# Performance work log

Hardware: AMD Instinct MI355X
Metric: run time of the kernel (lower is better)

## Reference

```python
import jax, jax.numpy as jnp
import numpy as np

N_HEAD = 8
D_HEAD = 64
D_MODEL = 512
CTX = 64
B = 2
Q_LEN = 2048
T = Q_LEN + CTX - 1


def setup_inputs() -> dict:
    key = jax.random.key(0)
    ks = jax.random.split(key, 7)
    HD = N_HEAD * D_HEAD
    return {
        "x": jax.random.normal(ks[0], (B, T, D_MODEL), jnp.float32),
        "r": jax.random.normal(ks[1], (CTX, D_MODEL), jnp.float32),
        "Wkv": jax.random.normal(ks[2], (D_MODEL, 2 * HD), jnp.float32) * 0.02,
        "Wq": jax.random.normal(ks[3], (D_MODEL, HD), jnp.float32) * 0.02,
        "bq": jax.random.normal(ks[4], (HD,), jnp.float32) * 0.02,
        "Wr": jax.random.normal(ks[5], (D_MODEL, HD), jnp.float32) * 0.02,
        "Wo": jax.random.normal(ks[6], (HD, D_MODEL), jnp.float32) * 0.02,
    }


def reference(x, r, Wkv, Wq, bq, Wr, Wo):
    Bb, Tt, _ = x.shape
    C = r.shape[0]
    H, Dh = N_HEAD, D_HEAD
    q_len = Tt - C + 1
    scale = Dh ** -0.5

    kv = x @ Wkv                                  # [B, T, 2*H*Dh]
    k_all = kv[..., : H * Dh].reshape(Bb, Tt, H, Dh)
    v_all = kv[..., H * Dh:].reshape(Bb, Tt, H, Dh)

    # sliding windows (torch unfold(1, ctx, 1) equivalent)
    idx = jnp.arange(q_len)[:, None] + jnp.arange(C)[None, :]   # [q, C]
    k_win = k_all[:, idx]                         # [B, q, C, H, Dh]
    v_win = v_all[:, idx]                         # [B, q, C, H, Dh]

    hq = (x[:, C - 1:] @ Wq + bq).reshape(Bb, q_len, H, Dh)     # [B, q, H, Dh]
    hr = (r @ Wr).reshape(C, H, Dh)                              # [C, H, Dh]

    # q . (k + r): split into content term + relative-position bias term
    scores = (jnp.einsum('bqhd,bqchd->bhqc', hq, k_win)
              + jnp.einsum('bqhd,chd->bhqc', hq, hr)) * scale    # [B, H, q, C]

    # padding mask: positions in first ctx-1 steps that are all-zero
    pad_mask = jnp.all(x[:, : C - 1] == 0, axis=-1)              # [B, C-1]
    full_mask = jnp.concatenate(
        [pad_mask, jnp.zeros((Bb, q_len), dtype=bool)], axis=1)  # [B, T]
    mask_win = full_mask[:, idx]                                 # [B, q, C]
    scores = jnp.where(mask_win[:, None], -jnp.inf, scores)

    w = jax.nn.softmax(scores, axis=-1)                          # [B, H, q, C]
    out = jnp.einsum('bhqc,bqchd->bqhd', w, v_win).reshape(Bb, q_len, H * Dh)
    return out @ Wo                                              # [B, q, d_model]
```

## Files before the change

kernel.cpp:

```cpp
#include <hip/hip_runtime.h>
#include <cstdint>
#include <cstddef>

#define NH 8
#define DH 64
#define DM 512
#define CTX 64
#define BB 2
#define QL 2048
#define TT (QL + CTX - 1)
#define HDIM 512
#define KVN 1024
#define KD 512

typedef unsigned short u16;
typedef __attribute__((ext_vector_type(8))) short bf16x8;
typedef __attribute__((ext_vector_type(4))) float f32x4;

__device__ __forceinline__ u16 f2bf(float f) {
    uint32_t u = __float_as_uint(f);
    u += 0x7FFF + ((u >> 16) & 1);
    return (u16)(u >> 16);
}
__device__ __forceinline__ float bf2f(u16 u) {
    return __uint_as_float((uint32_t)u << 16);
}

#define GLLDS(g, l) __builtin_amdgcn_global_load_lds( \
    (const __attribute__((address_space(1))) void*)(g), \
    (__attribute__((address_space(3))) void*)(l), 16, 0, 0)

__global__ __launch_bounds__(256) void prep_kernel(
    const float* __restrict__ x, const float* __restrict__ r,
    const float* __restrict__ Wkv, const float* __restrict__ Wq,
    const float* __restrict__ Wr, const float* __restrict__ Wo,
    u16* __restrict__ xb, u16* __restrict__ rb, u16* __restrict__ WkvqT,
    u16* __restrict__ WrT, u16* __restrict__ WoT, float* __restrict__ maskv)
{
    __shared__ float tile[64][65];
    __shared__ int anyflag;
    int bid = blockIdx.x;
    const int tid = threadIdx.x;

    if (bid < 2111) {
        int i = bid * 256 + tid;
        float4 v = ((const float4*)x)[i];
        ushort4 o; o.x = f2bf(v.x); o.y = f2bf(v.y); o.z = f2bf(v.z); o.w = f2bf(v.w);
        ((ushort4*)xb)[i] = o;
        return;
    }
    bid -= 2111;
    if (bid < 32) {
        int i = bid * 256 + tid;
        float4 v = ((const float4*)r)[i];
        ushort4 o; o.x = f2bf(v.x); o.y = f2bf(v.y); o.z = f2bf(v.z); o.w = f2bf(v.w);
        ((ushort4*)rb)[i] = o;
        return;
    }
    bid -= 32;
    if (bid >= 320) {
        int idx = bid - 320;
        int t = idx >> 1, b = idx & 1;
        const float* row = x + (size_t)(b * TT + t) * DM;
        bool nz = (row[tid] != 0.f) || (row[tid + 256] != 0.f);
        if (tid == 0) anyflag = 0;
        __syncthreads();
        unsigned long long bal = __ballot(nz);
        if ((tid & 63) == 0 && bal) atomicOr(&anyflag, 1);
        __syncthreads();
        if (tid == 0) maskv[b * 64 + t] = anyflag ? 0.f : -1e30f;
        return;
    }
    const float* W; u16* WT; int N; int tidx;
    if (bid < 128)      { W = Wkv; WT = WkvqT;                    N = 1024; tidx = bid; }
    else if (bid < 192) { W = Wq;  WT = WkvqT + (size_t)1024*512; N = 512;  tidx = bid - 128; }
    else if (bid < 256) { W = Wr;  WT = WrT;                      N = 512;  tidx = bid - 192; }
    else                { W = Wo;  WT = WoT;                      N = 512;  tidx = bid - 256; }
    const int tpr = N / 64;
    const int kb = (tidx / tpr) * 64, nb = (tidx % tpr) * 64;
    const int c4 = (tid & 15) * 4;
    for (int kk = tid >> 4; kk < 64; kk += 16) {
        float4 v = *(const float4*)&W[(size_t)(kb + kk) * N + nb + c4];
        tile[kk][c4 + 0] = v.x; tile[kk][c4 + 1] = v.y;
        tile[kk][c4 + 2] = v.z; tile[kk][c4 + 3] = v.w;
    }
    __syncthreads();
    for (int nn = tid >> 4; nn < 64; nn += 16) {
        ushort4 o;
        o.x = f2bf(tile[c4 + 0][nn]); o.y = f2bf(tile[c4 + 1][nn]);
        o.z = f2bf(tile[c4 + 2][nn]); o.w = f2bf(tile[c4 + 3][nn]);
        *(ushort4*)&WT[(size_t)(nb + nn) * KD + kb + c4] = o;
    }
}

__global__ __launch_bounds__(256) void gemm_mfma(
    const u16* __restrict__ A, const u16* __restrict__ BT,
    u16* __restrict__ C, u16* __restrict__ C2, const float* __restrict__ bq,
    int mode)
{
    __shared__ u16 As[128 * 32];
    __shared__ u16 Bs[128 * 32];

    const int tid  = threadIdx.x;
    const int lane = tid & 63;
    const int w    = tid >> 6;
    const int wm   = (w >> 1) * 64;
    const int wn   = (w & 1) * 64;
    const int m0   = blockIdx.y * 128;
    const int n0   = blockIdx.x * 128;

    const int am0 = tid >> 2;
    const int ak0 = (tid & 3) * 8;
    const u16* ga0 = A  + (size_t)(m0 + am0) * KD + ak0;
    const u16* ga1 = ga0 + (size_t)64 * KD;
    const u16* gb0 = BT + (size_t)(n0 + am0) * KD + ak0;
    const u16* gb1 = gb0 + (size_t)64 * KD;

    f32x4 acc[4][4];
#pragma unroll
    for (int i = 0; i < 4; i++)
#pragma unroll
        for (int j = 0; j < 4; j++)
            acc[i][j] = (f32x4){0.f, 0.f, 0.f, 0.f};

    for (int kt = 0; kt < KD; kt += 32) {
        __syncthreads();
        GLLDS(ga0 + kt, &As[(size_t)w * 512]);
        GLLDS(ga1 + kt, &As[2048 + (size_t)w * 512]);
        GLLDS(gb0 + kt, &Bs[(size_t)w * 512]);
        GLLDS(gb1 + kt, &Bs[2048 + (size_t)w * 512]);
        __syncthreads();

        const int fm = lane & 15;
        const int fk = (lane >> 4) * 8;
        bf16x8 af[4], bfr[4];
#pragma unroll
        for (int i = 0; i < 4; i++)
            af[i] = *(const bf16x8*)&As[(wm + i * 16 + fm) * 32 + fk];
#pragma unroll
        for (int j = 0; j < 4; j++)
            bfr[j] = *(const bf16x8*)&Bs[(wn + j * 16 + fm) * 32 + fk];
#pragma unroll
        for (int i = 0; i < 4; i++)
#pragma unroll
            for (int j = 0; j < 4; j++)
                acc[i][j] = __builtin_amdgcn_mfma_f32_16x16x32_bf16(af[i], bfr[j], acc[i][j], 0, 0, 0);
    }

    const int fc = lane & 15;
    const int fr = (lane >> 4) * 4;
    if (mode == 1) {
        const bool iskv = (n0 < 1024);
#pragma unroll
        for (int i = 0; i < 4; i++)
#pragma unroll
            for (int rr = 0; rr < 4; rr++) {
                int row = m0 + wm + i * 16 + fr + rr;
                if (row < BB * TT) {
                    if (iskv) {
#pragma unroll
                        for (int j = 0; j < 4; j++) {
                            int col = n0 + wn + j * 16 + fc;
                            C[(size_t)row * KVN + col] = f2bf(acc[i][j][rr]);
                        }
                    } else {
                        int bb = row / TT;
                        int t  = row - bb * TT;
                        if (t >= CTX - 1) {
                            size_t orow = (size_t)(bb * QL + t - (CTX - 1));
#pragma unroll
                            for (int j = 0; j < 4; j++) {
                                int col = n0 + wn + j * 16 + fc - 1024;
                                C2[orow * HDIM + col] = f2bf(acc[i][j][rr] + bq[col]);
                            }
                        }
                    }
                }
            }
    } else {
#pragma unroll
        for (int i = 0; i < 4; i++)
#pragma unroll
            for (int rr = 0; rr < 4; rr++) {
                int row = m0 + wm + i * 16 + fr + rr;
                if (row < CTX) {
#pragma unroll
                    for (int j = 0; j < 4; j++) {
                        int col = n0 + wn + j * 16 + fc;
                        C[(size_t)row * HDIM + col] = f2bf(acc[i][j][rr]);
                    }
                }
            }
    }
}

__global__ __launch_bounds__(256) void gemm_n64(
    const u16* __restrict__ A, const u16* __restrict__ BT,
    float* __restrict__ C, int M, int N)
{
    __shared__ u16 As[128 * 32];
    __shared__ u16 Bs[64 * 32];

    const int tid  = threadIdx.x;
    const int lane = tid & 63;
    const int w    = tid >> 6;
    const int wm   = (w >> 1) * 64;
    const int wn   = (w & 1) * 32;
    const int m0   = blockIdx.y * 128;
    const int n0   = blockIdx.x * 64;

    const int am0 = tid >> 2;
    const int ak0 = (tid & 3) * 8;
    const u16* ga0 = A  + (size_t)(m0 + am0) * KD + ak0;
    const u16* ga1 = ga0 + (size_t)64 * KD;
    const u16* gb0 = BT + (size_t)(n0 + am0) * KD + ak0;

    f32x4 acc[4][2];
#pragma unroll
    for (int i = 0; i < 4; i++)
#pragma unroll
        for (int j = 0; j < 2; j++)
            acc[i][j] = (f32x4){0.f, 0.f, 0.f, 0.f};

    for (int kt = 0; kt < KD; kt += 32) {
        __syncthreads();
        GLLDS(ga0 + kt, &As[(size_t)w * 512]);
        GLLDS(ga1 + kt, &As[2048 + (size_t)w * 512]);
        GLLDS(gb0 + kt, &Bs[(size_t)w * 512]);
        __syncthreads();

        const int fm = lane & 15;
        const int fk = (lane >> 4) * 8;
        bf16x8 af[4], bfr[2];
#pragma unroll
        for (int i = 0; i < 4; i++)
            af[i] = *(const bf16x8*)&As[(wm + i * 16 + fm) * 32 + fk];
#pragma unroll
        for (int j = 0; j < 2; j++)
            bfr[j] = *(const bf16x8*)&Bs[(wn + j * 16 + fm) * 32 + fk];
#pragma unroll
        for (int i = 0; i < 4; i++)
#pragma unroll
            for (int j = 0; j < 2; j++)
                acc[i][j] = __builtin_amdgcn_mfma_f32_16x16x32_bf16(af[i], bfr[j], acc[i][j], 0, 0, 0);
    }

    const int fc = lane & 15;
    const int fr = (lane >> 4) * 4;
#pragma unroll
    for (int i = 0; i < 4; i++)
#pragma unroll
        for (int rr = 0; rr < 4; rr++) {
            int row = m0 + wm + i * 16 + fr + rr;
            if (row < M) {
#pragma unroll
                for (int j = 0; j < 2; j++) {
                    int col = n0 + wn + j * 16 + fc;
                    C[(size_t)row * N + col] = acc[i][j][rr];
                }
            }
        }
}

__global__ __launch_bounds__(256) void attn_mfma(
    const u16* __restrict__ kvb, const u16* __restrict__ hqb,
    const u16* __restrict__ hrb, const float* __restrict__ maskv,
    u16* __restrict__ attnb)
{
    __shared__ __align__(16) char lds[55296];
    float* sprime = (float*)lds;
    u16*   vTs    = (u16*)lds;
    float* s2s    = (float*)(lds + 20480);
    u16*   wband  = (u16*)(lds + 37888);

    const int q0 = blockIdx.x * 64;
    const int h  = blockIdx.y;
    const int b  = blockIdx.z;
    const int tid  = threadIdx.x;
    const int lane = tid & 63;
    const int w    = tid >> 6;
    const int qb   = q0 + w * 16;

    {
        uint32_t* wz = (uint32_t*)wband;
#pragma unroll
        for (int i = 0; i < 17; i++) wz[tid + i * 256] = 0;
    }
    __syncthreads();

    const int fm = lane & 15;
    const int fk = (lane >> 4) * 8;

    const u16* hqrow = hqb + (size_t)(b * QL + qb + fm) * HDIM + h * DH + fk;
    bf16x8 afr0 = *(const bf16x8*)(hqrow);
    bf16x8 afr1 = *(const bf16x8*)(hqrow + 32);

    {
        const u16* kbase = kvb + (size_t)(b * TT + qb + fm) * KVN + h * DH + fk;
#pragma unroll
        for (int nt = 0; nt < 5; nt++) {
            bf16x8 b0 = *(const bf16x8*)(kbase + (size_t)nt * 16 * KVN);
            bf16x8 b1 = *(const bf16x8*)(kbase + (size_t)nt * 16 * KVN + 32);
            f32x4 acc = (f32x4){0.f, 0.f, 0.f, 0.f};
            acc = __builtin_amdgcn_mfma_f32_16x16x32_bf16(afr0, b0, acc, 0, 0, 0);
            acc = __builtin_amdgcn_mfma_f32_16x16x32_bf16(afr1, b1, acc, 0, 0, 0);
            const int row = (lane >> 4) * 4;
#pragma unroll
            for (int r = 0; r < 4; r++)
                sprime[w * 1280 + (row + r) * 80 + nt * 16 + fm] = acc[r];
        }
    }
    {
        const u16* hrbase = hrb + (size_t)fm * HDIM + h * DH + fk;
#pragma unroll
        for (int nc = 0; nc < 4; nc++) {
            bf16x8 b0 = *(const bf16x8*)(hrbase + (size_t)nc * 16 * HDIM);
            bf16x8 b1 = *(const bf16x8*)(hrbase + (size_t)nc * 16 * HDIM + 32);
            f32x4 acc = (f32x4){0.f, 0.f, 0.f, 0.f};
            acc = __builtin_amdgcn_mfma_f32_16x16x32_bf16(afr0, b0, acc, 0, 0, 0);
            acc = __builtin_amdgcn_mfma_f32_16x16x32_bf16(afr1, b1, acc, 0, 0, 0);
            const int row = (lane >> 4) * 4;
#pragma unroll
            for (int r = 0; r < 4; r++)
                s2s[w * 1088 + (row + r) * 68 + nc * 16 + fm] = acc[r];
        }
    }

#pragma unroll 1
    for (int i = 0; i < 16; i++) {
        const int qloc = w * 16 + i;
        float s = (sprime[w * 1280 + i * 80 + i + lane] +
                   s2s[w * 1088 + i * 68 + lane]) * 0.125f;
        if (q0 == 0) {
            int t = qloc + lane;
            if (t < 63) s += maskv[b * 64 + t];
        }
        float mx = s;
#pragma unroll
        for (int off = 32; off; off >>= 1) mx = fmaxf(mx, __shfl_xor(mx, off, 64));
        float e = __expf(s - mx);
        float sum = e;
#pragma unroll
        for (int off = 32; off; off >>= 1) sum += __shfl_xor(sum, off, 64);
        wband[qloc * 136 + qloc + lane] = f2bf(e / sum);
    }
    __syncthreads();

    {
        const int r0 = tid >> 4;
        const int c4 = (tid & 15) * 4;
        for (int rr = r0; rr < 127; rr += 16) {
            ushort4 vv = *(const ushort4*)&kvb[(size_t)(b * TT + q0 + rr) * KVN + HDIM + h * DH + c4];
            vTs[(c4 + 0) * 136 + rr] = vv.x;
            vTs[(c4 + 1) * 136 + rr] = vv.y;
            vTs[(c4 + 2) * 136 + rr] = vv.z;
            vTs[(c4 + 3) * 136 + rr] = vv.w;
        }
        if (tid < 64) vTs[tid * 136 + 127] = 0;
    }
    __syncthreads();

    f32x4 oacc[4];
#pragma unroll
    for (int j = 0; j < 4; j++) oacc[j] = (f32x4){0.f, 0.f, 0.f, 0.f};
#pragma unroll
    for (int ks = 0; ks < 4; ks++) {
        bf16x8 wa = *(const bf16x8*)&wband[(w * 16 + fm) * 136 + ks * 32 + fk];
#pragma unroll
        for (int j = 0; j < 4; j++) {
            bf16x8 vb = *(const bf16x8*)&vTs[(j * 16 + fm) * 136 + ks * 32 + fk];
            oacc[j] = __builtin_amdgcn_mfma_f32_16x16x32_bf16(wa, vb, oacc[j], 0, 0, 0);
        }
    }
    {
        const int row = (lane >> 4) * 4;
#pragma unroll
        for (int j = 0; j < 4; j++)
#pragma unroll
            for (int r = 0; r < 4; r++)
                attnb[(size_t)(b * QL + qb + row + r) * HDIM + h * DH + j * 16 + fm] =
                    f2bf(oacc[j][r]);
    }
}

extern "C" void kernel_launch(void* const* d_in, const int* in_sizes, int n_in,
                              void* d_out, int out_size, void* d_ws, size_t ws_size,
                              hipStream_t stream)
{
    const float* x   = (const float*)d_in[0];
    const float* r   = (const float*)d_in[1];
    const float* Wkv = (const float*)d_in[2];
    const float* Wq  = (const float*)d_in[3];
    const float* bq  = (const float*)d_in[4];
    const float* Wr  = (const float*)d_in[5];
    const float* Wo  = (const float*)d_in[6];
    float* out = (float*)d_out;

    char* p = (char*)d_ws;
    u16* xb     = (u16*)p;  p += (size_t)4224 * 512 * 2;
    u16* rb     = (u16*)p;  p += (size_t)128 * 512 * 2;
    u16* WkvqT  = (u16*)p;  p += (size_t)1536 * 512 * 2;
    u16* WrT    = (u16*)p;  p += (size_t)512 * 512 * 2;
    u16* WoT    = (u16*)p;  p += (size_t)512 * 512 * 2;
    u16* kvb    = (u16*)p;  p += (size_t)4224 * 1024 * 2;
    u16* hqb    = (u16*)p;  p += (size_t)4096 * 512 * 2;
    u16* hrb    = (u16*)p;  p += (size_t)64 * 512 * 2;
    u16* attnb  = (u16*)p;  p += (size_t)4096 * 512 * 2;
    float* maskv = (float*)p;

    hipLaunchKernelGGL(prep_kernel, dim3(2589), dim3(256), 0, stream,
                       x, r, Wkv, Wq, Wr, Wo, xb, rb, WkvqT, WrT, WoT, maskv);
    hipLaunchKernelGGL(gemm_mfma, dim3(1536 / 128, 33), dim3(256), 0, stream,
                       xb, WkvqT, kvb, hqb, bq, 1);
    hipLaunchKernelGGL(gemm_mfma, dim3(512 / 128, 1), dim3(256), 0, stream,
                       rb, WrT, hrb, nullptr, nullptr, 2);
    hipLaunchKernelGGL(attn_mfma, dim3(QL / 64, NH, BB), dim3(256), 0, stream,
                       kvb, hqb, hrb, maskv, attnb);
    hipLaunchKernelGGL(gemm_n64, dim3(512 / 64, 4096 / 128), dim3(256), 0, stream,
                       attnb, WoT, out, 4096, 512);
}
```

Measured before the change: 133.6 us.

## Fuse all stages into one persistent cooperative kernel with grid syncs

Replaces the five separate launches (prep, QKV GEMM, hr GEMM, attention, output GEMM) with a single cooperative persistent kernel. Work is spread over blocks in grid-stride loops, and stages are separated by grid-wide barriers. The projection GEMM now uses a 128x64 tile instead of 128x128, which gives more work units to balance across the persistent grid, and the hr GEMM is folded into the same stage. The aim is to remove launch gaps and per-kernel tail effects. In exchange it pays for grid-sync overhead, and every stage runs at the occupancy allowed by the attention stage's 55 KB LDS footprint.

```diff
diff --git a/kernel.cpp b/kernel.cpp
--- a/kernel.cpp
+++ b/kernel.cpp
@@ -1,4 +1,5 @@
 #include <hip/hip_runtime.h>
+#include <hip/hip_cooperative_groups.h>
 #include <cstdint>
 #include <cstddef>
 
@@ -22,128 +23,61 @@
     u += 0x7FFF + ((u >> 16) & 1);
     return (u16)(u >> 16);
 }
-__device__ __forceinline__ float bf2f(u16 u) {
-    return __uint_as_float((uint32_t)u << 16);
-}
 
 #define GLLDS(g, l) __builtin_amdgcn_global_load_lds( \
     (const __attribute__((address_space(1))) void*)(g), \
     (__attribute__((address_space(3))) void*)(l), 16, 0, 0)
 
-__global__ __launch_bounds__(256) void prep_kernel(
-    const float* __restrict__ x, const float* __restrict__ r,
-    const float* __restrict__ Wkv, const float* __restrict__ Wq,
-    const float* __restrict__ Wr, const float* __restrict__ Wo,
-    u16* __restrict__ xb, u16* __restrict__ rb, u16* __restrict__ WkvqT,
-    u16* __restrict__ WrT, u16* __restrict__ WoT, float* __restrict__ maskv)
-{
-    __shared__ float tile[64][65];
-    __shared__ int anyflag;
-    int bid = blockIdx.x;
-    const int tid = threadIdx.x;
-
-    if (bid < 2111) {
-        int i = bid * 256 + tid;
-        float4 v = ((const float4*)x)[i];
-        ushort4 o; o.x = f2bf(v.x); o.y = f2bf(v.y); o.z = f2bf(v.z); o.w = f2bf(v.w);
-        ((ushort4*)xb)[i] = o;
-        return;
-    }
-    bid -= 2111;
-    if (bid < 32) {
-        int i = bid * 256 + tid;
-        float4 v = ((const float4*)r)[i];
-        ushort4 o; o.x = f2bf(v.x); o.y = f2bf(v.y); o.z = f2bf(v.z); o.w = f2bf(v.w);
-        ((ushort4*)rb)[i] = o;
-        return;
-    }
-    bid -= 32;
-    if (bid >= 320) {
-        int idx = bid - 320;
-        int t = idx >> 1, b = idx & 1;
-        const float* row = x + (size_t)(b * TT + t) * DM;
-        bool nz = (row[tid] != 0.f) || (row[tid + 256] != 0.f);
-        if (tid == 0) anyflag = 0;
-        __syncthreads();
-        unsigned long long bal = __ballot(nz);
-        if ((tid & 63) == 0 && bal) atomicOr(&anyflag, 1);
-        __syncthreads();
-        if (tid == 0) maskv[b * 64 + t] = anyflag ? 0.f : -1e30f;
-        return;
-    }
-    const float* W; u16* WT; int N; int tidx;
-    if (bid < 128)      { W = Wkv; WT = WkvqT;                    N = 1024; tidx = bid; }
-    else if (bid < 192) { W = Wq;  WT = WkvqT + (size_t)1024*512; N = 512;  tidx = bid - 128; }
-    else if (bid < 256) { W = Wr;  WT = WrT;                      N = 512;  tidx = bid - 192; }
-    else                { W = Wo;  WT = WoT;                      N = 512;  tidx = bid - 256; }
-    const int tpr = N / 64;
-    const int kb = (tidx / tpr) * 64, nb = (tidx % tpr) * 64;
-    const int c4 = (tid & 15) * 4;
-    for (int kk = tid >> 4; kk < 64; kk += 16) {
-        float4 v = *(const float4*)&W[(size_t)(kb + kk) * N + nb + c4];
-        tile[kk][c4 + 0] = v.x; tile[kk][c4 + 1] = v.y;
-        tile[kk][c4 + 2] = v.z; tile[kk][c4 + 3] = v.w;
-    }
-    __syncthreads();
-    for (int nn = tid >> 4; nn < 64; nn += 16) {
-        ushort4 o;
-        o.x = f2bf(tile[c4 + 0][nn]); o.y = f2bf(tile[c4 + 1][nn]);
-        o.z = f2bf(tile[c4 + 2][nn]); o.w = f2bf(tile[c4 + 3][nn]);
-        *(ushort4*)&WT[(size_t)(nb + nn) * KD + kb + c4] = o;
-    }
-}
-
-__global__ __launch_bounds__(256) void gemm_mfma(
+struct Ptrs {
+    const float *x, *r, *Wkv, *Wq, *bq, *Wr, *Wo;
+    float* outp;
+    u16 *xb, *rb, *WkvqT, *WrT, *WoT, *kvb, *hqb, *hrb, *attnb;
+    float* maskv;
+};
+
+__device__ __forceinline__ void gemm_unit(
     const u16* __restrict__ A, const u16* __restrict__ BT,
-    u16* __restrict__ C, u16* __restrict__ C2, const float* __restrict__ bq,
-    int mode)
-{
-    __shared__ u16 As[128 * 32];
-    __shared__ u16 Bs[128 * 32];
-
-    const int tid  = threadIdx.x;
+    int m0, int n0, char* smem, int tid, int mode, const Ptrs& p)
+{
+    u16* As = (u16*)smem;
+    u16* Bs = (u16*)(smem + 8192);
     const int lane = tid & 63;
     const int w    = tid >> 6;
     const int wm   = (w >> 1) * 64;
-    const int wn   = (w & 1) * 64;
-    const int m0   = blockIdx.y * 128;
-    const int n0   = blockIdx.x * 128;
-
-    const int am0 = tid >> 2;
-    const int ak0 = (tid & 3) * 8;
-    const u16* ga0 = A  + (size_t)(m0 + am0) * KD + ak0;
+    const int wn   = (w & 1) * 32;
+
+    const u16* ga0 = A  + (size_t)(m0 + (tid >> 2)) * KD + (tid & 3) * 8;
     const u16* ga1 = ga0 + (size_t)64 * KD;
-    const u16* gb0 = BT + (size_t)(n0 + am0) * KD + ak0;
-    const u16* gb1 = gb0 + (size_t)64 * KD;
-
-    f32x4 acc[4][4];
+    const u16* gb0 = BT + (size_t)(n0 + (tid >> 2)) * KD + (tid & 3) * 8;
+
+    f32x4 acc[4][2];
 #pragma unroll
     for (int i = 0; i < 4; i++)
 #pragma unroll
-        for (int j = 0; j < 4; j++)
+        for (int j = 0; j < 2; j++)
             acc[i][j] = (f32x4){0.f, 0.f, 0.f, 0.f};
+
+    const int fm = lane & 15;
+    const int fk = (lane >> 4) * 8;
 
     for (int kt = 0; kt < KD; kt += 32) {
         __syncthreads();
-        GLLDS(ga0 + kt, &As[(size_t)w * 512]);
-        GLLDS(ga1 + kt, &As[2048 + (size_t)w * 512]);
-        GLLDS(gb0 + kt, &Bs[(size_t)w * 512]);
-        GLLDS(gb1 + kt, &Bs[2048 + (size_t)w * 512]);
+        GLLDS(ga0 + kt, As + w * 512);
+        GLLDS(ga1 + kt, As + 2048 + w * 512);
+        GLLDS(gb0 + kt, Bs + w * 512);
         __syncthreads();
 
-        const int fm = lane & 15;
-        const int fk = (lane >> 4) * 8;
-        bf16x8 af[4], bfr[4];
+        bf16x8 af[4], bfr[2];
 #pragma unroll
         for (int i = 0; i < 4; i++)
             af[i] = *(const bf16x8*)&As[(wm + i * 16 + fm) * 32 + fk];
 #pragma unroll
-        for (int j = 0; j < 4; j++)
+        for (int j = 0; j < 2; j++)
             bfr[j] = *(const bf16x8*)&Bs[(wn + j * 16 + fm) * 32 + fk];
 #pragma unroll
         for (int i = 0; i < 4; i++)
 #pragma unroll
-            for (int j = 0; j < 4; j++)
+            for (int j = 0; j < 2; j++)
                 acc[i][j] = __builtin_amdgcn_mfma_f32_16x16x32_bf16(af[i], bfr[j], acc[i][j], 0, 0, 0);
     }
 
@@ -159,9 +93,9 @@
                 if (row < BB * TT) {
                     if (iskv) {
 #pragma unroll
-                        for (int j = 0; j < 4; j++) {
+                        for (int j = 0; j < 2; j++) {
                             int col = n0 + wn + j * 16 + fc;
-                            C[(size_t)row * KVN + col] = f2bf(acc[i][j][rr]);
+                            p.kvb[(size_t)row * KVN + col] = f2bf(acc[i][j][rr]);
                         }
                     } else {
                         int bb = row / TT;
@@ -169,15 +103,15 @@
                         if (t >= CTX - 1) {
                             size_t orow = (size_t)(bb * QL + t - (CTX - 1));
 #pragma unroll
-                            for (int j = 0; j < 4; j++) {
+                            for (int j = 0; j < 2; j++) {
                                 int col = n0 + wn + j * 16 + fc - 1024;
-                                C2[orow * HDIM + col] = f2bf(acc[i][j][rr] + bq[col]);
+                                p.hqb[orow * HDIM + col] = f2bf(acc[i][j][rr] + p.bq[col]);
                             }
                         }
                     }
                 }
             }
-    } else {
+    } else if (mode == 2) {
 #pragma unroll
         for (int i = 0; i < 4; i++)
 #pragma unroll
@@ -185,102 +119,109 @@
                 int row = m0 + wm + i * 16 + fr + rr;
                 if (row < CTX) {
 #pragma unroll
-                    for (int j = 0; j < 4; j++) {
+                    for (int j = 0; j < 2; j++) {
                         int col = n0 + wn + j * 16 + fc;
-                        C[(size_t)row * HDIM + col] = f2bf(acc[i][j][rr]);
+                        p.hrb[(size_t)row * HDIM + col] = f2bf(acc[i][j][rr]);
                     }
                 }
             }
-    }
-}
-
-__global__ __launch_bounds__(256) void gemm_n64(
-    const u16* __restrict__ A, const u16* __restrict__ BT,
-    float* __restrict__ C, int M, int N)
-{
-    __shared__ u16 As[128 * 32];
-    __shared__ u16 Bs[64 * 32];
-
-    const int tid  = threadIdx.x;
-    const int lane = tid & 63;
-    const int w    = tid >> 6;
-    const int wm   = (w >> 1) * 64;
-    const int wn   = (w & 1) * 32;
-    const int m0   = blockIdx.y * 128;
-    const int n0   = blockIdx.x * 64;
-
-    const int am0 = tid >> 2;
-    const int ak0 = (tid & 3) * 8;
-    const u16* ga0 = A  + (size_t)(m0 + am0) * KD + ak0;
-    const u16* ga1 = ga0 + (size_t)64 * KD;
-    const u16* gb0 = BT + (size_t)(n0 + am0) * KD + ak0;
-
-    f32x4 acc[4][2];
-#pragma unroll
-    for (int i = 0; i < 4; i++)
-#pragma unroll
-        for (int j = 0; j < 2; j++)
-            acc[i][j] = (f32x4){0.f, 0.f, 0.f, 0.f};
-
-    for (int kt = 0; kt < KD; kt += 32) {
-        __syncthreads();
-        GLLDS(ga0 + kt, &As[(size_t)w * 512]);
-        GLLDS(ga1 + kt, &As[2048 + (size_t)w * 512]);
-        GLLDS(gb0 + kt, &Bs[(size_t)w * 512]);
-        __syncthreads();
-
-        const int fm = lane & 15;
-        const int fk = (lane >> 4) * 8;
-        bf16x8 af[4], bfr[2];
+    } else {
 #pragma unroll
         for (int i = 0; i < 4; i++)
-            af[i] = *(const bf16x8*)&As[(wm + i * 16 + fm) * 32 + fk];
-#pragma unroll
-        for (int j = 0; j < 2; j++)
-            bfr[j] = *(const bf16x8*)&Bs[(wn + j * 16 + fm) * 32 + fk];
-#pragma unroll
-        for (int i = 0; i < 4; i++)
-#pragma unroll
-            for (int j = 0; j < 2; j++)
-                acc[i][j] = __builtin_amdgcn_mfma_f32_16x16x32_bf16(af[i], bfr[j], acc[i][j], 0, 0, 0);
-    }
-
-    const int fc = lane & 15;
-    const int fr = (lane >> 4) * 4;
-#pragma unroll
-    for (int i = 0; i < 4; i++)
-#pragma unroll
-        for (int rr = 0; rr < 4; rr++) {
-            int row = m0 + wm + i * 16 + fr + rr;
-            if (row < M) {
+#pragma unroll
+            for (int rr = 0; rr < 4; rr++) {
+                int row = m0 + wm + i * 16 + fr + rr;
 #pragma unroll
                 for (int j = 0; j < 2; j++) {
                     int col = n0 + wn + j * 16 + fc;
-                    C[(size_t)row * N + col] = acc[i][j][rr];
+                    p.outp[(size_t)row * DM + col] = acc[i][j][rr];
                 }
             }
-        }
-}
-
-__global__ __launch_bounds__(256) void attn_mfma(
-    const u16* __restrict__ kvb, const u16* __restrict__ hqb,
-    const u16* __restrict__ hrb, const float* __restrict__ maskv,
-    u16* __restrict__ attnb)
-{
-    __shared__ __align__(16) char lds[55296];
-    float* sprime = (float*)lds;
-    u16*   vTs    = (u16*)lds;
-    float* s2s    = (float*)(lds + 20480);
-    u16*   wband  = (u16*)(lds + 37888);
-
-    const int q0 = blockIdx.x * 64;
-    const int h  = blockIdx.y;
-    const int b  = blockIdx.z;
-    const int tid  = threadIdx.x;
+    }
+}
+
+__device__ __forceinline__ void stageA(int u, int tid, char* smem, const Ptrs& p)
+{
+    int bid = u;
+    if (bid < 2111) {
+        int i = bid * 256 + tid;
+        float4 v = ((const float4*)p.x)[i];
+        ushort4 o; o.x = f2bf(v.x); o.y = f2bf(v.y); o.z = f2bf(v.z); o.w = f2bf(v.w);
+        ((ushort4*)p.xb)[i] = o;
+        return;
+    }
+    bid -= 2111;
+    if (bid < 32) {
+        int i = bid * 256 + tid;
+        float4 v = ((const float4*)p.r)[i];
+        ushort4 o; o.x = f2bf(v.x); o.y = f2bf(v.y); o.z = f2bf(v.z); o.w = f2bf(v.w);
+        ((ushort4*)p.rb)[i] = o;
+        return;
+    }
+    bid -= 32;
+    if (bid >= 320) {
+        int* anyflag = (int*)(smem + 16896);
+        int idx = bid - 320;
+        int t = idx >> 1, b = idx & 1;
+        const float* row = p.x + (size_t)(b * TT + t) * DM;
+        bool nz = (row[tid] != 0.f) || (row[tid + 256] != 0.f);
+        if (tid == 0) *anyflag = 0;
+        __syncthreads();
+        unsigned long long bal = __ballot(nz);
+        if ((tid & 63) == 0 && bal) atomicOr(anyflag, 1);
+        __syncthreads();
+        if (tid == 0) p.maskv[b * 64 + t] = *anyflag ? 0.f : -1e30f;
+        return;
+    }
+    float (*tile)[65] = (float(*)[65])smem;
+    const float* W; u16* WT; int N; int tidx;
+    if (bid < 128)      { W = p.Wkv; WT = p.WkvqT;                      N = 1024; tidx = bid; }
+    else if (bid < 192) { W = p.Wq;  WT = p.WkvqT + (size_t)1024 * 512; N = 512;  tidx = bid - 128; }
+    else if (bid < 256) { W = p.Wr;  WT = p.WrT;                        N = 512;  tidx = bid - 192; }
+    else                { W = p.Wo;  WT = p.WoT;                        N = 512;  tidx = bid - 256; }
+    const int tpr = N / 64;
+    const int kb = (tidx / tpr) * 64, nbo = (tidx % tpr) * 64;
+    const int c4 = (tid & 15) * 4;
+    __syncthreads();
+    for (int kk = tid >> 4; kk < 64; kk += 16) {
+        float4 v = *(const float4*)&W[(size_t)(kb + kk) * N + nbo + c4];
+        tile[kk][c4 + 0] = v.x; tile[kk][c4 + 1] = v.y;
+        tile[kk][c4 + 2] = v.z; tile[kk][c4 + 3] = v.w;
+    }
+    __syncthreads();
+    for (int nn = tid >> 4; nn < 64; nn += 16) {
+        ushort4 o;
+        o.x = f2bf(tile[c4 + 0][nn]); o.y = f2bf(tile[c4 + 1][nn]);
+        o.z = f2bf(tile[c4 + 2][nn]); o.w = f2bf(tile[c4 + 3][nn]);
+        *(ushort4*)&WT[(size_t)(nbo + nn) * KD + kb + c4] = o;
+    }
+}
+
+__device__ __forceinline__ void stageB(int u, int tid, char* smem, const Ptrs& p)
+{
+    if (u < 792) {
+        int mu = u / 24, nu = u - mu * 24;
+        gemm_unit(p.xb, p.WkvqT, mu * 128, nu * 64, smem, tid, 1, p);
+    } else {
+        gemm_unit(p.rb, p.WrT, 0, (u - 792) * 64, smem, tid, 2, p);
+    }
+}
+
+__device__ __forceinline__ void stageC(int u, int tid, char* smem, const Ptrs& p)
+{
+    float* sprime = (float*)smem;
+    u16*   vTs    = (u16*)smem;
+    float* s2s    = (float*)(smem + 20480);
+    u16*   wband  = (u16*)(smem + 37888);
+
+    const int q0 = (u & 31) * 64;
+    const int h  = (u >> 5) & 7;
+    const int b  = u >> 8;
     const int lane = tid & 63;
     const int w    = tid >> 6;
     const int qb   = q0 + w * 16;
 
+    __syncthreads();
     {
         uint32_t* wz = (uint32_t*)wband;
 #pragma unroll
@@ -291,12 +232,12 @@
     const int fm = lane & 15;
     const int fk = (lane >> 4) * 8;
 
-    const u16* hqrow = hqb + (size_t)(b * QL + qb + fm) * HDIM + h * DH + fk;
+    const u16* hqrow = p.hqb + (size_t)(b * QL + qb + fm) * HDIM + h * DH + fk;
     bf16x8 afr0 = *(const bf16x8*)(hqrow);
     bf16x8 afr1 = *(const bf16x8*)(hqrow + 32);
 
     {
-        const u16* kbase = kvb + (size_t)(b * TT + qb + fm) * KVN + h * DH + fk;
+        const u16* kbase = p.kvb + (size_t)(b * TT + qb + fm) * KVN + h * DH + fk;
 #pragma unroll
         for (int nt = 0; nt < 5; nt++) {
             bf16x8 b0 = *(const bf16x8*)(kbase + (size_t)nt * 16 * KVN);
@@ -306,12 +247,12 @@
             acc = __builtin_amdgcn_mfma_f32_16x16x32_bf16(afr1, b1, acc, 0, 0, 0);
             const int row = (lane >> 4) * 4;
 #pragma unroll
-            for (int r = 0; r < 4; r++)
-                sprime[w * 1280 + (row + r) * 80 + nt * 16 + fm] = acc[r];
+            for (int rr = 0; rr < 4; rr++)
+                sprime[w * 1280 + (row + rr) * 80 + nt * 16 + fm] = acc[rr];
         }
     }
     {
-        const u16* hrbase = hrb + (size_t)fm * HDIM + h * DH + fk;
+        const u16* hrbase = p.hrb + (size_t)fm * HDIM + h * DH + fk;
 #pragma unroll
         for (int nc = 0; nc < 4; nc++) {
             bf16x8 b0 = *(const bf16x8*)(hrbase + (size_t)nc * 16 * HDIM);
@@ -321,8 +262,8 @@
             acc = __builtin_amdgcn_mfma_f32_16x16x32_bf16(afr1, b1, acc, 0, 0, 0);
             const int row = (lane >> 4) * 4;
 #pragma unroll
-            for (int r = 0; r < 4; r++)
-                s2s[w * 1088 + (row + r) * 68 + nc * 16 + fm] = acc[r];
+            for (int rr = 0; rr < 4; rr++)
+                s2s[w * 1088 + (row + rr) * 68 + nc * 16 + fm] = acc[rr];
         }
     }
 
@@ -333,7 +274,7 @@
                    s2s[w * 1088 + i * 68 + lane]) * 0.125f;
         if (q0 == 0) {
             int t = qloc + lane;
-            if (t < 63) s += maskv[b * 64 + t];
+            if (t < 63) s += p.maskv[b * 64 + t];
         }
         float mx = s;
 #pragma unroll
@@ -350,7 +291,7 @@
         const int r0 = tid >> 4;
         const int c4 = (tid & 15) * 4;
         for (int rr = r0; rr < 127; rr += 16) {
-            ushort4 vv = *(const ushort4*)&kvb[(size_t)(b * TT + q0 + rr) * KVN + HDIM + h * DH + c4];
+            ushort4 vv = *(const ushort4*)&p.kvb[(size_t)(b * TT + q0 + rr) * KVN + HDIM + h * DH + c4];
             vTs[(c4 + 0) * 136 + rr] = vv.x;
             vTs[(c4 + 1) * 136 + rr] = vv.y;
             vTs[(c4 + 2) * 136 + rr] = vv.z;
@@ -377,45 +318,96 @@
 #pragma unroll
         for (int j = 0; j < 4; j++)
 #pragma unroll
-            for (int r = 0; r < 4; r++)
-                attnb[(size_t)(b * QL + qb + row + r) * HDIM + h * DH + j * 16 + fm] =
-                    f2bf(oacc[j][r]);
-    }
+            for (int rr = 0; rr < 4; rr++)
+                p.attnb[(size_t)(b * QL + qb + row + rr) * HDIM + h * DH + j * 16 + fm] =
+                    f2bf(oacc[j][rr]);
+    }
+}
+
+__device__ __forceinline__ void stageD(int u, int tid, char* smem, const Ptrs& p)
+{
+    gemm_unit(p.attnb, p.WoT, (u >> 3) * 128, (u & 7) * 64, smem, tid, 3, p);
+}
+
+__global__ __launch_bounds__(256, 2) void fused_all(Ptrs p)
+{
+    __shared__ __align__(16) char smem[55296];
+    cooperative_groups::grid_group gg = cooperative_groups::this_grid();
+    const int tid = threadIdx.x;
+    const int nb  = gridDim.x;
+
+    for (int u = blockIdx.x; u < 2589; u += nb) stageA(u, tid, smem, p);
+    __threadfence(); gg.sync();
+    for (int u = blockIdx.x; u < 800; u += nb)  stageB(u, tid, smem, p);
+    __threadfence(); gg.sync();
+    for (int u = blockIdx.x; u < 512; u += nb)  stageC(u, tid, smem, p);
+    __threadfence(); gg.sync();
+    for (int u = blockIdx.x; u < 256; u += nb)  stageD(u, tid, smem, p);
+}
+
+__global__ __launch_bounds__(256) void k_prep(Ptrs p)
+{
+    __shared__ __align__(16) char smem[16912];
+    stageA(blockIdx.x, threadIdx.x, smem, p);
+}
+__global__ __launch_bounds__(256) void k_gB(Ptrs p)
+{
+    __shared__ __align__(16) char smem[12288];
+    stageB(blockIdx.x, threadIdx.x, smem, p);
+}
+__global__ __launch_bounds__(256, 2) void k_attn(Ptrs p)
+{
+    __shared__ __align__(16) char smem[55296];
+    stageC(blockIdx.x, threadIdx.x, smem, p);
+}
+__global__ __launch_bounds__(256) void k_gD(Ptrs p)
+{
+    __shared__ __align__(16) char smem[12288];
+    stageD(blockIdx.x, threadIdx.x, smem, p);
 }
 
 extern "C" void kernel_launch(void* const* d_in, const int* in_sizes, int n_in,
                               void* d_out, int out_size, void* d_ws, size_t ws_size,
                               hipStream_t stream)
 {
-    const float* x   = (const float*)d_in[0];
-    const float* r   = (const float*)d_in[1];
-    const float* Wkv = (const float*)d_in[2];
-    const float* Wq  = (const float*)d_in[3];
-    const float* bq  = (const float*)d_in[4];
-    const float* Wr  = (const float*)d_in[5];
-    const float* Wo  = (const float*)d_in[6];
-    float* out = (float*)d_out;
-
-    char* p = (char*)d_ws;
-    u16* xb     = (u16*)p;  p += (size_t)4224 * 512 * 2;
-    u16* rb     = (u16*)p;  p += (size_t)128 * 512 * 2;
-    u16* WkvqT  = (u16*)p;  p += (size_t)1536 * 512 * 2;
-    u16* WrT    = (u16*)p;  p += (size_t)512 * 512 * 2;
-    u16* WoT    = (u16*)p;  p += (size_t)512 * 512 * 2;
-    u16* kvb    = (u16*)p;  p += (size_t)4224 * 1024 * 2;
-    u16* hqb    = (u16*)p;  p += (size_t)4096 * 512 * 2;
-    u16* hrb    = (u16*)p;  p += (size_t)64 * 512 * 2;
-    u16* attnb  = (u16*)p;  p += (size_t)4096 * 512 * 2;
-    float* maskv = (float*)p;
-
-    hipLaunchKernelGGL(prep_kernel, dim3(2589), dim3(256), 0, stream,
-                       x, r, Wkv, Wq, Wr, Wo, xb, rb, WkvqT, WrT, WoT, maskv);
-    hipLaunchKernelGGL(gemm_mfma, dim3(1536 / 128, 33), dim3(256), 0, stream,
-                       xb, WkvqT, kvb, hqb, bq, 1);
-    hipLaunchKernelGGL(gemm_mfma, dim3(512 / 128, 1), dim3(256), 0, stream,
-                       rb, WrT, hrb, nullptr, nullptr, 2);
-    hipLaunchKernelGGL(attn_mfma, dim3(QL / 64, NH, BB), dim3(256), 0, stream,
-                       kvb, hqb, hrb, maskv, attnb);
-    hipLaunchKernelGGL(gemm_n64, dim3(512 / 64, 4096 / 128), dim3(256), 0, stream,
-                       attnb, WoT, out, 4096, 512);
-}
+    Ptrs p;
+    p.x   = (const float*)d_in[0];
+    p.r   = (const float*)d_in[1];
+    p.Wkv = (const float*)d_in[2];
+    p.Wq  = (const float*)d_in[3];
+    p.bq  = (const float*)d_in[4];
+    p.Wr  = (const float*)d_in[5];
+    p.Wo  = (const float*)d_in[6];
+    p.outp = (float*)d_out;
+
+    char* w = (char*)d_ws;
+    p.xb    = (u16*)w;  w += (size_t)4224 * 512 * 2;
+    p.rb    = (u16*)w;  w += (size_t)128 * 512 * 2;
+    p.WkvqT = (u16*)w;  w += (size_t)1536 * 512 * 2;
+    p.WrT   = (u16*)w;  w += (size_t)512 * 512 * 2;
+    p.WoT   = (u16*)w;  w += (size_t)512 * 512 * 2;
+    p.kvb   = (u16*)w;  w += (size_t)4224 * 1024 * 2;
+    p.hqb   = (u16*)w;  w += (size_t)4096 * 512 * 2;
+    p.hrb   = (u16*)w;  w += (size_t)64 * 512 * 2;
+    p.attnb = (u16*)w;  w += (size_t)4096 * 512 * 2;
+    p.maskv = (float*)w;
+
+    int bpc = 0;
+    hipError_t err = hipOccupancyMaxActiveBlocksPerMultiprocessor(
+        &bpc, reinterpret_cast<const void*>(fused_all), 256, 0);
+    bool ok = (err == hipSuccess && bpc >= 1);
+    if (ok) {
+        int grid = bpc * 256;
+        if (grid > 512) grid = 512;
+        void* kargs[] = { (void*)&p };
+        err = hipLaunchCooperativeKernel(reinterpret_cast<const void*>(fused_all),
+                                         dim3(grid), dim3(256), kargs, 0, stream);
+        ok = (err == hipSuccess);
+    }
+    if (!ok) {
+        hipLaunchKernelGGL(k_prep, dim3(2589), dim3(256), 0, stream, p);
+        hipLaunchKernelGGL(k_gB,   dim3(800),  dim3(256), 0, stream, p);
+        hipLaunchKernelGGL(k_attn, dim3(512),  dim3(256), 0, stream, p);
+        hipLaunchKernelGGL(k_gD,   dim3(256),  dim3(256), 0, stream, p);
+    }
+}
```

Measured after the change: 336.5 us. 152% more time.
